# Kernel tuning notes

Measured on AMD Instinct MI355X. Metric: run time of the kernel, lower is better.

The kernel has to match this reference:

```python
import jax, jax.numpy as jnp
import numpy as np

B, C, H, W = 16, 512, 64, 64
NH = 8  # num_heads


def setup_inputs() -> dict:
    key = jax.random.key(0)
    ks = jax.random.split(key, 7)
    s = 1.0 / np.sqrt(C)
    return {
        "x": jax.random.normal(ks[0], (B, C, H, W), dtype=jnp.float32),
        "wq": jax.random.normal(ks[1], (C, C), dtype=jnp.float32) * s,
        "bq": jax.random.normal(ks[2], (C,), dtype=jnp.float32) * 0.01,
        "wk": jax.random.normal(ks[3], (C, C), dtype=jnp.float32) * s,
        "bk": jax.random.normal(ks[4], (C,), dtype=jnp.float32) * 0.01,
        "wv": jax.random.normal(ks[5], (C, C), dtype=jnp.float32) * s,
        "bv": jax.random.normal(ks[6], (C,), dtype=jnp.float32) * 0.01,
    }


def reference(x, wq, bq, wk, bk, wv, bv):
    b, c_in, h, w = x.shape
    hd = c_in // NH  # head dim

    def conv1x1(wt, bias):
        # 1x1 conv == channel GEMM: (b,c,h,w) x (o,c) -> (b,o,h,w)
        y = jnp.einsum("bchw,oc->bohw", x, wt) + bias[None, :, None, None]
        # view(b, nh, hd, h, w).permute(0,1,3,4,2) -> (b, nh, h, w, hd)
        return y.reshape(b, NH, hd, h, w).transpose(0, 1, 3, 4, 2)

    q = conv1x1(wq, bq)
    k = conv1x1(wk, bk)
    v = conv1x1(wv, bv)

    # attention along the width axis, per (batch, head, row)
    energy = jnp.einsum("bnhqc,bnhkc->bnhqk", q, k)  # (b,nh,h,w,w)
    attn = jax.nn.softmax(energy, axis=-1)
    out = jnp.einsum("bnhqk,bnhkc->bnhqc", attn, v)  # (b,nh,h,w,hd)

    # permute(0,1,4,2,3) -> (b,nh,hd,h,w) -> view(b, C, h, w)
    out = out.transpose(0, 1, 4, 2, 3).reshape(b, c_in, h, w)
    return out + x
```

## Files before the change

### kernel.cpp

```cpp
#include <hip/hip_runtime.h>
#include <stdint.h>

#define B_   16
#define C_   512
#define H_   64
#define W_   64
#define NH_  8
#define HD_  64
#define HW_  4096

typedef __attribute__((ext_vector_type(8))) _Float16 f16x8;
typedef __attribute__((ext_vector_type(8))) unsigned short u16x8;
typedef __attribute__((ext_vector_type(4))) unsigned short u16x4;
typedef __attribute__((ext_vector_type(4))) float f32x4;

static __device__ __forceinline__ unsigned short f2h(float f) {
  _Float16 h = (_Float16)f;
  unsigned short u;
  __builtin_memcpy(&u, &h, 2);
  return u;
}

static __device__ __forceinline__ void gld_lds16(const void* g, void* l) {
  __builtin_amdgcn_global_load_lds((__attribute__((address_space(1))) void*)g,
                                   (__attribute__((address_space(3))) void*)l,
                                   16, 0, 0);
}

__global__ __launch_bounds__(256) void rcca_cvtw(const float* __restrict__ wq,
                                                 const float* __restrict__ wk,
                                                 const float* __restrict__ wv,
                                                 unsigned short* __restrict__ Wc) {
  const int i = blockIdx.x * 256 + threadIdx.x;
  const int e = i * 4;
  const float* w = (e < 262144) ? wq : (e < 524288) ? wk : wv;
  const int off = e & 262143;
  const float4 v = *(const float4*)(w + off);
  u16x4 p;
  p[0] = f2h(v.x); p[1] = f2h(v.y); p[2] = f2h(v.z); p[3] = f2h(v.w);
  *(u16x4*)(Wc + e) = p;
}

__global__ __launch_bounds__(256) void rcca_fused(
    const float* __restrict__ x, const unsigned short* __restrict__ Wc,
    const float* __restrict__ bq, const float* __restrict__ bk, const float* __restrict__ bv,
    float* __restrict__ out) {
  __shared__ __align__(16) char smem[73728];
  unsigned short* lA = (unsigned short*)smem;
  unsigned short* lB = (unsigned short*)(smem + 16384);
  float* sX = (float*)(smem + 40960);
  const int sbid = blockIdx.x;
  const int lg = ((sbid & 7) << 9) | (sbid >> 3);
  const int head = lg & 7;
  const int bh = lg >> 3;
  const int b = bh >> 5;
  const int ht = bh & 31;
  const int t = threadIdx.x;
  const int wid = t >> 6, lane = t & 63, r = lane & 15, q = lane >> 4;
  const int rx = r & 7;
  const int wm = wid >> 1, wn = wid & 1;
  const int arow = t >> 3;
  const int acol = ((t & 7) ^ (arow & 7)) * 8;
  char* lBb = (char*)lB;
  char* sXb = (char*)sX;
  const int wbase = wid * 1024;
  const int xc = t >> 5;
  const int xch = t & 31;
  const float* Xbase = x + (size_t)b * C_ * HW_ + (size_t)ht * 128;
  const unsigned short* Bbase = Wc + (size_t)head * 64 * C_;
  const int thw = t >> 1, thalf = t & 1;
  f32x4 acc[4][6];
#pragma unroll
  for (int i = 0; i < 4; ++i)
#pragma unroll
    for (int j = 0; j < 6; ++j) acc[i][j] = (f32x4){0.f, 0.f, 0.f, 0.f};

  for (int k0 = 0; k0 < C_; k0 += 64) {
    __syncthreads();
#pragma unroll
    for (int rr = 0; rr < 8; ++rr) {
      const int c = rr * 8 + xc;
      gld_lds16(Xbase + (size_t)(k0 + c) * HW_ + xch * 4, sXb + rr * 4096 + wbase);
    }
#pragma unroll
    for (int p = 0; p < 6; ++p) {
      const size_t grow = (size_t)((p >> 1) * 512 + (p & 1) * 32 + arow) * C_;
      gld_lds16(Bbase + grow + k0 + acol, lBb + p * 4096 + wbase);
    }
    __syncthreads();
#pragma unroll
    for (int u = 0; u < 4; ++u) {
      const int chunk = thalf * 4 + u;
      u16x8 pk;
#pragma unroll
      for (int j = 0; j < 8; ++j)
        pk[j] = f2h(sX[(chunk * 8 + j) * 128 + thw]);
      *(u16x8*)&lA[thw * 64 + ((chunk ^ (thw & 7)) * 8)] = pk;
    }
    __syncthreads();
#pragma unroll
    for (int kk = 0; kk < 64; kk += 32) {
      const int cb = ((kk >> 3) + q) ^ rx;
      f16x8 av[4], bw[6];
#pragma unroll
      for (int i = 0; i < 4; ++i)
        av[i] = *(const f16x8*)&lA[(wm * 64 + i * 16 + r) * 64 + cb * 8];
#pragma unroll
      for (int j = 0; j < 6; ++j)
        bw[j] = *(const f16x8*)&lB[(wn * 96 + j * 16 + r) * 64 + cb * 8];
#pragma unroll
      for (int i = 0; i < 4; ++i)
#pragma unroll
        for (int j = 0; j < 6; ++j)
          acc[i][j] = __builtin_amdgcn_mfma_f32_16x16x32_f16(av[i], bw[j], acc[i][j], 0, 0, 0);
    }
  }
  __syncthreads();
  unsigned short* sQh = (unsigned short*)(smem + wm * 27648);
  unsigned short* sKh = (unsigned short*)(smem + wm * 27648 + 9216);
  unsigned short* sVh = (unsigned short*)(smem + wm * 27648 + 18432);
#pragma unroll
  for (int j = 0; j < 6; ++j) {
    const int n0 = wn * 96 + j * 16;
    const int sel = n0 >> 6;
    const int dd = (n0 & 63) + r;
    const float* bias = (sel == 0) ? bq : (sel == 1) ? bk : bv;
    const float bias_v = bias[head * 64 + dd];
    if (sel < 2) {
      unsigned short* dst = (sel == 0) ? sQh : sKh;
#pragma unroll
      for (int i = 0; i < 4; ++i)
#pragma unroll
        for (int reg = 0; reg < 4; ++reg)
          dst[(i * 16 + q * 4 + reg) * 72 + dd] = f2h(acc[i][j][reg] + bias_v);
    } else {
#pragma unroll
      for (int i = 0; i < 4; ++i) {
        u16x4 pk;
#pragma unroll
        for (int reg = 0; reg < 4; ++reg) pk[reg] = f2h(acc[i][j][reg] + bias_v);
        *(u16x4*)&sVh[dd * 72 + i * 16 + q * 4] = pk;
      }
    }
  }
  __syncthreads();
  unsigned short* sPh = (unsigned short*)(smem + 55296 + wm * 9216);
  f32x4 s2[2][4];
#pragma unroll
  for (int i2 = 0; i2 < 2; ++i2)
#pragma unroll
    for (int j = 0; j < 4; ++j) s2[i2][j] = (f32x4){0.f, 0.f, 0.f, 0.f};
#pragma unroll
  for (int kk = 0; kk < 64; kk += 32) {
    f16x8 aq0 = *(const f16x8*)&sQh[(wn * 32 + r) * 72 + kk + q * 8];
    f16x8 aq1 = *(const f16x8*)&sQh[(wn * 32 + 16 + r) * 72 + kk + q * 8];
#pragma unroll
    for (int j = 0; j < 4; ++j) {
      f16x8 bk8 = *(const f16x8*)&sKh[(j * 16 + r) * 72 + kk + q * 8];
      s2[0][j] = __builtin_amdgcn_mfma_f32_16x16x32_f16(aq0, bk8, s2[0][j], 0, 0, 0);
      s2[1][j] = __builtin_amdgcn_mfma_f32_16x16x32_f16(aq1, bk8, s2[1][j], 0, 0, 0);
    }
  }
  float inv2[2][4];
#pragma unroll
  for (int i2 = 0; i2 < 2; ++i2)
#pragma unroll
    for (int reg = 0; reg < 4; ++reg) {
      float mx = fmaxf(fmaxf(s2[i2][0][reg], s2[i2][1][reg]),
                       fmaxf(s2[i2][2][reg], s2[i2][3][reg]));
#pragma unroll
      for (int o = 1; o < 16; o <<= 1) mx = fmaxf(mx, __shfl_xor(mx, o, 64));
      float p0 = __expf(s2[i2][0][reg] - mx);
      float p1 = __expf(s2[i2][1][reg] - mx);
      float p2 = __expf(s2[i2][2][reg] - mx);
      float p3 = __expf(s2[i2][3][reg] - mx);
      float sum = p0 + p1 + p2 + p3;
#pragma unroll
      for (int o = 1; o < 16; o <<= 1) sum += __shfl_xor(sum, o, 64);
      inv2[i2][reg] = 1.0f / sum;
      const int row = wn * 32 + i2 * 16 + q * 4 + reg;
      sPh[row * 72 + r] = f2h(p0);
      sPh[row * 72 + 16 + r] = f2h(p1);
      sPh[row * 72 + 32 + r] = f2h(p2);
      sPh[row * 72 + 48 + r] = f2h(p3);
    }
  __syncthreads();
  f32x4 o4[2][4];
#pragma unroll
  for (int i2 = 0; i2 < 2; ++i2)
#pragma unroll
    for (int jd = 0; jd < 4; ++jd) o4[i2][jd] = (f32x4){0.f, 0.f, 0.f, 0.f};
#pragma unroll
  for (int kk = 0; kk < 64; kk += 32) {
    f16x8 ap0 = *(const f16x8*)&sPh[(wn * 32 + r) * 72 + kk + q * 8];
    f16x8 ap1 = *(const f16x8*)&sPh[(wn * 32 + 16 + r) * 72 + kk + q * 8];
#pragma unroll
    for (int jd = 0; jd < 4; ++jd) {
      f16x8 bv8 = *(const f16x8*)&sVh[(jd * 16 + r) * 72 + kk + q * 8];
      o4[0][jd] = __builtin_amdgcn_mfma_f32_16x16x32_f16(ap0, bv8, o4[0][jd], 0, 0, 0);
      o4[1][jd] = __builtin_amdgcn_mfma_f32_16x16x32_f16(ap1, bv8, o4[1][jd], 0, 0, 0);
    }
  }
  float* sOh = (float*)(smem + wm * 27648);
#pragma unroll
  for (int i2 = 0; i2 < 2; ++i2)
#pragma unroll
    for (int jd = 0; jd < 4; ++jd) {
      const int d = jd * 16 + r;
#pragma unroll
      for (int reg = 0; reg < 4; ++reg) {
        const int w = wn * 32 + i2 * 16 + q * 4 + reg;
        sOh[d * 66 + w] = o4[i2][jd][reg] * inv2[i2][reg];
      }
    }
  __syncthreads();
  const int d = t >> 2, w0 = (t & 3) * 16;
#pragma unroll
  for (int hs = 0; hs < 2; ++hs) {
    const float* sO2 = (const float*)(smem + hs * 27648);
    const int h = ht * 2 + hs;
    const size_t obase = (((size_t)b * C_ + head * 64 + d) * H_ + h) * (size_t)W_ + w0;
    const float4* xr = (const float4*)(x + obase);
    float4* op = (float4*)(out + obase);
#pragma unroll
    for (int u = 0; u < 4; ++u) {
      float4 xv = xr[u];
      float4 ov;
      ov.x = sO2[d * 66 + w0 + u * 4 + 0] + xv.x;
      ov.y = sO2[d * 66 + w0 + u * 4 + 1] + xv.y;
      ov.z = sO2[d * 66 + w0 + u * 4 + 2] + xv.z;
      ov.w = sO2[d * 66 + w0 + u * 4 + 3] + xv.w;
      op[u] = ov;
    }
  }
}

extern "C" void kernel_launch(void* const* d_in, const int* in_sizes, int n_in,
                              void* d_out, int out_size, void* d_ws, size_t ws_size,
                              hipStream_t stream) {
  const float* x  = (const float*)d_in[0];
  const float* wq = (const float*)d_in[1];
  const float* bq = (const float*)d_in[2];
  const float* wk = (const float*)d_in[3];
  const float* bk = (const float*)d_in[4];
  const float* wv = (const float*)d_in[5];
  const float* bv = (const float*)d_in[6];
  float* out = (float*)d_out;
  char* ws = (char*)d_ws;
  unsigned short* Wc = (unsigned short*)ws;
  hipLaunchKernelGGL(rcca_cvtw,  dim3(768),  dim3(256), 0, stream, wq, wk, wv, Wc);
  hipLaunchKernelGGL(rcca_fused, dim3(4096), dim3(256), 0, stream, x, Wc, bq, bk, bv, out);
}
```

Baseline: 425.3 us.

## Load weight fragments directly from global and prefetch next X tile during compute

Each wave now reads its fp16 weight B-fragments straight from global memory into registers, so the LDS staging buffer for weights is no longer filled. The async global-to-LDS load of the next x chunk is issued after the current chunk has been converted to fp16, letting it overlap with the MFMA work. The goal is fewer LDS round trips and fewer barriers per k-step, plus hiding x load latency. In exchange it uses more registers, and the global weight reads rely on L2 hits; each lane fetches 16-byte strided pieces, so coalescing is worse.

```diff
diff --git a/kernel.cpp b/kernel.cpp
--- a/kernel.cpp
+++ b/kernel.cpp
@@ -47,7 +47,6 @@
     float* __restrict__ out) {
   __shared__ __align__(16) char smem[73728];
   unsigned short* lA = (unsigned short*)smem;
-  unsigned short* lB = (unsigned short*)(smem + 16384);
   float* sX = (float*)(smem + 40960);
   const int sbid = blockIdx.x;
   const int lg = ((sbid & 7) << 9) | (sbid >> 3);
@@ -59,15 +58,18 @@
   const int wid = t >> 6, lane = t & 63, r = lane & 15, q = lane >> 4;
   const int rx = r & 7;
   const int wm = wid >> 1, wn = wid & 1;
-  const int arow = t >> 3;
-  const int acol = ((t & 7) ^ (arow & 7)) * 8;
-  char* lBb = (char*)lB;
   char* sXb = (char*)sX;
   const int wbase = wid * 1024;
   const int xc = t >> 5;
   const int xch = t & 31;
   const float* Xbase = x + (size_t)b * C_ * HW_ + (size_t)ht * 128;
-  const unsigned short* Bbase = Wc + (size_t)head * 64 * C_;
+  const unsigned short* rowp[6];
+#pragma unroll
+  for (int j = 0; j < 6; ++j) {
+    const int n = wn * 96 + j * 16 + r;
+    const int sel = n >> 6, dloc = n & 63;
+    rowp[j] = Wc + (size_t)(sel * 512 + head * 64 + dloc) * C_;
+  }
   const int thw = t >> 1, thalf = t & 1;
   f32x4 acc[4][6];
 #pragma unroll
@@ -75,18 +77,12 @@
 #pragma unroll
     for (int j = 0; j < 6; ++j) acc[i][j] = (f32x4){0.f, 0.f, 0.f, 0.f};
 
-  for (int k0 = 0; k0 < C_; k0 += 64) {
-    __syncthreads();
-#pragma unroll
-    for (int rr = 0; rr < 8; ++rr) {
-      const int c = rr * 8 + xc;
-      gld_lds16(Xbase + (size_t)(k0 + c) * HW_ + xch * 4, sXb + rr * 4096 + wbase);
-    }
-#pragma unroll
-    for (int p = 0; p < 6; ++p) {
-      const size_t grow = (size_t)((p >> 1) * 512 + (p & 1) * 32 + arow) * C_;
-      gld_lds16(Bbase + grow + k0 + acol, lBb + p * 4096 + wbase);
-    }
+#pragma unroll
+  for (int rr = 0; rr < 8; ++rr)
+    gld_lds16(Xbase + (size_t)(rr * 8 + xc) * HW_ + xch * 4, sXb + rr * 4096 + wbase);
+
+  for (int tt = 0; tt < 8; ++tt) {
+    const int k0 = tt * 64;
     __syncthreads();
 #pragma unroll
     for (int u = 0; u < 4; ++u) {
@@ -98,21 +94,30 @@
       *(u16x8*)&lA[thw * 64 + ((chunk ^ (thw & 7)) * 8)] = pk;
     }
     __syncthreads();
-#pragma unroll
-    for (int kk = 0; kk < 64; kk += 32) {
-      const int cb = ((kk >> 3) + q) ^ rx;
-      f16x8 av[4], bw[6];
+    f16x8 bw[6][2];
+#pragma unroll
+    for (int j = 0; j < 6; ++j)
+#pragma unroll
+      for (int kx = 0; kx < 2; ++kx)
+        bw[j][kx] = *(const f16x8*)(rowp[j] + k0 + kx * 32 + q * 8);
+    if (tt < 7) {
+#pragma unroll
+      for (int rr = 0; rr < 8; ++rr)
+        gld_lds16(Xbase + (size_t)(k0 + 64 + rr * 8 + xc) * HW_ + xch * 4,
+                  sXb + rr * 4096 + wbase);
+    }
+#pragma unroll
+    for (int kx = 0; kx < 2; ++kx) {
+      const int cb = (kx * 4 + q) ^ rx;
+      f16x8 av[4];
 #pragma unroll
       for (int i = 0; i < 4; ++i)
         av[i] = *(const f16x8*)&lA[(wm * 64 + i * 16 + r) * 64 + cb * 8];
 #pragma unroll
-      for (int j = 0; j < 6; ++j)
-        bw[j] = *(const f16x8*)&lB[(wn * 96 + j * 16 + r) * 64 + cb * 8];
-#pragma unroll
       for (int i = 0; i < 4; ++i)
 #pragma unroll
         for (int j = 0; j < 6; ++j)
-          acc[i][j] = __builtin_amdgcn_mfma_f32_16x16x32_f16(av[i], bw[j], acc[i][j], 0, 0, 0);
+          acc[i][j] = __builtin_amdgcn_mfma_f32_16x16x32_f16(av[i], bw[j][kx], acc[i][j], 0, 0, 0);
     }
   }
   __syncthreads();
```

After: 724.7 us. 1.7x slower.
